# Performance work log

Measured on AMD Instinct MI355X. Metric: run time of the kernel, lower is better.

The kernel has to match this reference:

```python
import jax, jax.numpy as jnp
import numpy as np

H = 16  # num_heads
D = 1024  # hidden_size

def setup_inputs() -> dict:
    key = jax.random.key(0)
    ks = jax.random.split(key, 9)
    s = 1.0 / np.sqrt(D).astype(np.float32)
    return {
        'x':  jax.random.normal(ks[0], (2, 2048, D), dtype=jnp.float32),
        'wq': jax.random.normal(ks[1], (D, D), dtype=jnp.float32) * s,
        'bq': jax.random.normal(ks[2], (D,), dtype=jnp.float32) * s,
        'wk': jax.random.normal(ks[3], (D, D), dtype=jnp.float32) * s,
        'bk': jax.random.normal(ks[4], (D,), dtype=jnp.float32) * s,
        'wv': jax.random.normal(ks[5], (D, D), dtype=jnp.float32) * s,
        'bv': jax.random.normal(ks[6], (D,), dtype=jnp.float32) * s,
        'wo': jax.random.normal(ks[7], (D, D), dtype=jnp.float32) * s,
        'bo': jax.random.normal(ks[8], (D,), dtype=jnp.float32) * s,
    }

def _split_heads(t):
    # [b, s, (h d)] -> [b, h, s, d]
    b, s, _ = t.shape
    return t.reshape(b, s, H, D // H).transpose(0, 2, 1, 3)

def reference(x, wq, bq, wk, bk, wv, bv, wo, bo):
    q = _split_heads(x @ wq + bq)  # [b, h, s, d]
    k = _split_heads(x @ wk + bk)
    v = _split_heads(x @ wv + bv)
    scale = 1.0 / jnp.sqrt(jnp.asarray(q.shape[-1], q.dtype))
    attn = jnp.einsum('bhqd,bhkd->bhqk', q, k) * scale
    attn = jax.nn.softmax(attn, axis=-1)
    o = jnp.einsum('bhqk,bhkd->bhqd', attn, v)
    b, h, s, d = o.shape
    o = o.transpose(0, 2, 1, 3).reshape(b, s, h * d)  # concat heads
    return o @ wo + bo
```

## Files before the change

### kernel.cpp

```cpp
#include <hip/hip_runtime.h>
#include <stdint.h>
#include <stddef.h>


typedef __bf16 bf16_t;
typedef __bf16 bf16x8 __attribute__((ext_vector_type(8)));
typedef __bf16 bf16x4 __attribute__((ext_vector_type(4)));
typedef __bf16 bf16x2 __attribute__((ext_vector_type(2)));
typedef float  f32x4  __attribute__((ext_vector_type(4)));
typedef float  f32x8  __attribute__((ext_vector_type(8)));
typedef float  f32x16 __attribute__((ext_vector_type(16)));
typedef uint32_t u32x4 __attribute__((ext_vector_type(4)));

static constexpr float kQScale = 0.18033688011112042f;

__device__ __forceinline__ void gload_lds16(const bf16_t* g, bf16_t* l) {
  __builtin_amdgcn_global_load_lds((__attribute__((address_space(1))) void*)(void*)g,
                                   (__attribute__((address_space(3))) void*)l, 16, 0, 0);
}

__device__ __forceinline__ uint32_t pk_bf16(float lo, float hi) {
  bf16x2 v; v[0] = (bf16_t)lo; v[1] = (bf16_t)hi;
  return __builtin_bit_cast(uint32_t, v);
}

__global__ __launch_bounds__(256) void prep_k(
    const float* __restrict__ x, bf16_t* __restrict__ xb,
    const float* __restrict__ wq, const float* __restrict__ wk,
    const float* __restrict__ wv, const float* __restrict__ wo,
    bf16_t* __restrict__ wqkvT, bf16_t* __restrict__ woT) {
  __shared__ float t[64][65];
  const int z = blockIdx.z;
  if (z == 4) {
    const int blk = blockIdx.y * 16 + blockIdx.x;
#pragma unroll
    for (int c = 0; c < 16; ++c) {
      const int i = c * 65536 + blk * 256 + threadIdx.x;
      float4 v = ((const float4*)x)[i];
      bf16x4 o;
      o[0] = (bf16_t)v.x; o[1] = (bf16_t)v.y; o[2] = (bf16_t)v.z; o[3] = (bf16_t)v.w;
      ((bf16x4*)xb)[i] = o;
    }
    return;
  }
  const float* src = z == 0 ? wq : z == 1 ? wk : z == 2 ? wv : wo;
  bf16_t* dst = z < 3 ? wqkvT + (size_t)z * 1024 * 1024 : woT;
  int n0 = blockIdx.x * 64, k0 = blockIdx.y * 64;
  int c = threadIdx.x & 63, r4 = threadIdx.x >> 6;
#pragma unroll
  for (int i = 0; i < 16; ++i) {
    int r = r4 + i * 4;
    t[r][c] = src[(size_t)(k0 + r) * 1024 + (n0 + c)];
  }
  __syncthreads();
#pragma unroll
  for (int i = 0; i < 16; ++i) {
    int r = r4 + i * 4;
    dst[(size_t)(n0 + r) * 1024 + (k0 + c)] = (bf16_t)t[c][r];
  }
}

__global__ __launch_bounds__(256) void gemm_qkv_k(
    const bf16_t* __restrict__ A, const bf16_t* __restrict__ Bw,
    bf16_t* __restrict__ Qb, bf16_t* __restrict__ Kb, bf16_t* __restrict__ Vt,
    const float* __restrict__ bq, const float* __restrict__ bk, const float* __restrict__ bv) {
  __shared__ alignas(16) bf16_t As[128 * 32];
  __shared__ alignas(16) bf16_t Bs[128 * 32];
  const int tid = threadIdx.x;
  const int lane = tid & 63;
  const int w = tid >> 6, wr = w >> 1, wc = w & 1;
  const int brow = blockIdx.y * 128, bcol = blockIdx.x * 128;
  const int l15 = lane & 15, ko = (lane >> 4) * 8;

  f32x4 acc[4][4] = {};
  const bf16_t* Ab = A + (size_t)brow * 1024;
  const bf16_t* Bb = Bw + (size_t)bcol * 1024;

  const int e0 = tid * 8;
  const int r0 = e0 >> 5, c0 = e0 & 31;

  for (int k0 = 0; k0 < 1024; k0 += 32) {
    gload_lds16(Ab + (size_t)r0 * 1024 + k0 + c0, &As[e0]);
    gload_lds16(Ab + (size_t)(r0 + 64) * 1024 + k0 + c0, &As[e0 + 2048]);
    gload_lds16(Bb + (size_t)r0 * 1024 + k0 + c0, &Bs[e0]);
    gload_lds16(Bb + (size_t)(r0 + 64) * 1024 + k0 + c0, &Bs[e0 + 2048]);
    __syncthreads();
    bf16x8 af[4], bfg[4];
#pragma unroll
    for (int i = 0; i < 4; ++i)
      af[i] = *(const bf16x8*)&As[(wr * 64 + i * 16 + l15) * 32 + ko];
#pragma unroll
    for (int i = 0; i < 4; ++i)
      bfg[i] = *(const bf16x8*)&Bs[(wc * 64 + i * 16 + l15) * 32 + ko];
#pragma unroll
    for (int i = 0; i < 4; ++i)
#pragma unroll
      for (int j = 0; j < 4; ++j)
        acc[i][j] = __builtin_amdgcn_mfma_f32_16x16x32_bf16(af[i], bfg[j], acc[i][j], 0, 0, 0);
    __syncthreads();
  }

  const int mat = bcol >> 10;
#pragma unroll
  for (int i = 0; i < 4; ++i) {
    const int gm0 = brow + wr * 64 + i * 16 + ((lane >> 4) << 2);
    const int b = gm0 >> 11, s0 = gm0 & 2047;
#pragma unroll
    for (int j = 0; j < 4; ++j) {
      const int gn = bcol + wc * 64 + j * 16 + l15;
      const int col = gn & 1023;
      const int h = col >> 6, dd = col & 63;
      if (mat == 2) {
        const float bsv = bv[col];
        bf16x4 pk;
#pragma unroll
        for (int r = 0; r < 4; ++r) pk[r] = (bf16_t)(acc[i][j][r] + bsv);
        *(bf16x4*)&Vt[(((size_t)b * 16 + h) * 64 + dd) * 2048 + s0] = pk;
      } else {
        bf16_t* dst = mat == 0 ? Qb : Kb;
        const float bsv = (mat == 0 ? bq : bk)[col];
        const float scl = mat == 0 ? kQScale : 1.0f;
#pragma unroll
        for (int r = 0; r < 4; ++r)
          dst[((((size_t)b * 16 + h) * 2048 + (s0 + r)) * 64 + dd)] = (bf16_t)((acc[i][j][r] + bsv) * scl);
      }
    }
  }
}

__global__ __launch_bounds__(256) void gemm_out_k(
    const bf16_t* __restrict__ A, const bf16_t* __restrict__ Bw,
    float* __restrict__ outF, const float* __restrict__ bo) {
  __shared__ alignas(16) bf16_t As[128 * 32];
  __shared__ alignas(16) bf16_t Bs[64 * 32];
  const int tid = threadIdx.x;
  const int lane = tid & 63;
  const int w = tid >> 6;
  const int brow = blockIdx.y * 128, bcol = blockIdx.x * 64;
  const int l15 = lane & 15, ko = (lane >> 4) * 8;

  f32x4 acc[2][4] = {};
  const bf16_t* Ab = A + (size_t)brow * 1024;
  const bf16_t* Bb = Bw + (size_t)bcol * 1024;

  const int e0 = tid * 8;
  const int r0 = e0 >> 5, c0 = e0 & 31;

  for (int k0 = 0; k0 < 1024; k0 += 32) {
    gload_lds16(Ab + (size_t)r0 * 1024 + k0 + c0, &As[e0]);
    gload_lds16(Ab + (size_t)(r0 + 64) * 1024 + k0 + c0, &As[e0 + 2048]);
    gload_lds16(Bb + (size_t)r0 * 1024 + k0 + c0, &Bs[e0]);
    __syncthreads();
    bf16x8 af[2], bfg[4];
#pragma unroll
    for (int i = 0; i < 2; ++i)
      af[i] = *(const bf16x8*)&As[(w * 32 + i * 16 + l15) * 32 + ko];
#pragma unroll
    for (int j = 0; j < 4; ++j)
      bfg[j] = *(const bf16x8*)&Bs[(j * 16 + l15) * 32 + ko];
#pragma unroll
    for (int i = 0; i < 2; ++i)
#pragma unroll
      for (int j = 0; j < 4; ++j)
        acc[i][j] = __builtin_amdgcn_mfma_f32_16x16x32_bf16(af[i], bfg[j], acc[i][j], 0, 0, 0);
    __syncthreads();
  }

#pragma unroll
  for (int i = 0; i < 2; ++i) {
    const int gm0 = brow + w * 32 + i * 16 + ((lane >> 4) << 2);
#pragma unroll
    for (int j = 0; j < 4; ++j) {
      const int gn = bcol + j * 16 + l15;
      const float bsv = bo[gn];
#pragma unroll
      for (int r = 0; r < 4; ++r)
        outF[(size_t)(gm0 + r) * 1024 + gn] = acc[i][j][r] + bsv;
    }
  }
}

__global__ __launch_bounds__(512) void attn_k(
    const bf16_t* __restrict__ Qb, const bf16_t* __restrict__ Kb,
    const bf16_t* __restrict__ Vt, bf16_t* __restrict__ O) {
  __shared__ alignas(16) bf16_t Ksm[2][2][4096];
  __shared__ alignas(16) bf16_t Vsm[2][2][4096];
  const int tid = threadIdx.x, lane = tid & 63, w = tid >> 6;
  const int l31 = lane & 31, hi = lane >> 5;
  const int qsub = w & 3, half = w >> 2;
  const int work = (blockIdx.x & 7) * 32 + (blockIdx.x >> 3);
  const int bh = work >> 3;
  const int q0 = (work & 7) * 256 + qsub * 64;

  const bf16_t* Qp = Qb + ((size_t)bh * 2048 + q0) * 64;

  const int chunk0 = qsub * 64 + lane;
  const int srow = chunk0 >> 3;
  const int swzc = (chunk0 & 7) ^ (srow & 7);
  const char* srcK0 = (const char*)(Kb + ((size_t)bh * 2048 + half * 1024) * 64) + srow * 128 + swzc * 16;
  const char* srcK1 = srcK0 + 32 * 128;
  const char* srcV0 = (const char*)(Vt + (size_t)bh * 64 * 2048 + half * 1024) + srow * 4096 + swzc * 16;
  const char* srcV1 = srcV0 + 32 * 4096;

  auto stage = [&](int buf) {
    bf16_t* kb = &Ksm[half][buf][qsub * 512];
    bf16_t* vb = &Vsm[half][buf][qsub * 512];
    gload_lds16((const bf16_t*)srcK0, kb);
    gload_lds16((const bf16_t*)srcK1, kb + 2048);
    gload_lds16((const bf16_t*)srcV0, vb);
    gload_lds16((const bf16_t*)srcV1, vb + 2048);
    srcK0 += 8192; srcK1 += 8192;
    srcV0 += 128;  srcV1 += 128;
  };

  const int xorv = l31 & 7;
  const bf16_t* kcb[4];
#pragma unroll
  for (int j = 0; j < 4; ++j) {
    const int co = ((j * 2 + hi) ^ xorv) * 8;
    kcb[j] = &Ksm[half][0][l31 * 64 + co];
  }
  const bf16_t* vptr[8];
#pragma unroll
  for (int c = 0; c < 8; ++c)
    vptr[c] = &Vsm[half][0][l31 * 64 + ((c ^ xorv) << 3) + 4 * hi];

  bf16x8 qf[2][4];
#pragma unroll
  for (int qb = 0; qb < 2; ++qb)
#pragma unroll
    for (int ds = 0; ds < 4; ++ds)
      qf[qb][ds] = *(const bf16x8*)&Qp[(size_t)(qb * 32 + l31) * 64 + ds * 16 + hi * 8];

  f32x16 oA0 = {}, oA1 = {}, oB0 = {}, oB1 = {};
  f32x16 lsA = {}, lsB = {};
  const f32x16 kz = {};

  auto exp_pack = [&](f32x16& s0, f32x16& s1, f32x16& lsum,
                      uint32_t* pw0, uint32_t* pw1) {
#pragma unroll
    for (int r = 0; r < 16; ++r) {
      s0[r] = __builtin_amdgcn_exp2f(s0[r]);
      s1[r] = __builtin_amdgcn_exp2f(s1[r]);
    }
    lsum += s0;
    lsum += s1;
#pragma unroll
    for (int g = 0; g < 4; ++g) {
      pw0[g * 2 + 0] = pk_bf16(s0[4 * g + 0], s0[4 * g + 1]);
      pw0[g * 2 + 1] = pk_bf16(s0[4 * g + 2], s0[4 * g + 3]);
      pw1[g * 2 + 0] = pk_bf16(s1[4 * g + 0], s1[4 * g + 1]);
      pw1[g * 2 + 1] = pk_bf16(s1[4 * g + 2], s1[4 * g + 3]);
    }
  };

  auto tile_body = [&](int buf) {
    const int bo = buf * 4096;
    bf16x8 kf0[4], kf1[4];
#pragma unroll
    for (int ds = 0; ds < 4; ++ds) {
      kf0[ds] = *(const bf16x8*)(kcb[ds] + bo);
      kf1[ds] = *(const bf16x8*)(kcb[ds] + bo + 2048);
    }
    __builtin_amdgcn_s_setprio(1);
    f32x16 sA0 = __builtin_amdgcn_mfma_f32_32x32x16_bf16(kf0[0], qf[0][0], kz, 0, 0, 0);
    f32x16 sB0 = __builtin_amdgcn_mfma_f32_32x32x16_bf16(kf0[0], qf[1][0], kz, 0, 0, 0);
    f32x16 sA1 = __builtin_amdgcn_mfma_f32_32x32x16_bf16(kf1[0], qf[0][0], kz, 0, 0, 0);
    f32x16 sB1 = __builtin_amdgcn_mfma_f32_32x32x16_bf16(kf1[0], qf[1][0], kz, 0, 0, 0);
#pragma unroll
    for (int ds = 1; ds < 4; ++ds) {
      sA0 = __builtin_amdgcn_mfma_f32_32x32x16_bf16(kf0[ds], qf[0][ds], sA0, 0, 0, 0);
      sB0 = __builtin_amdgcn_mfma_f32_32x32x16_bf16(kf0[ds], qf[1][ds], sB0, 0, 0, 0);
      sA1 = __builtin_amdgcn_mfma_f32_32x32x16_bf16(kf1[ds], qf[0][ds], sA1, 0, 0, 0);
      sB1 = __builtin_amdgcn_mfma_f32_32x32x16_bf16(kf1[ds], qf[1][ds], sB1, 0, 0, 0);
    }
    __builtin_amdgcn_s_setprio(0);

    uint32_t pwA0[8], pwA1[8], pwB0[8], pwB1[8];
    exp_pack(sA0, sA1, lsA, pwA0, pwA1);
    exp_pack(sB0, sB1, lsB, pwB0, pwB1);

#pragma unroll
    for (int st = 0; st < 2; ++st) {
#pragma unroll
      for (int ks = 0; ks < 2; ++ks) {
        const bf16_t* pA = vptr[4 * st + 2 * ks] + bo;
        const bf16_t* pB = vptr[4 * st + 2 * ks + 1] + bo;
        const bf16x4 a0 = *(const bf16x4*)pA;
        const bf16x4 a1 = *(const bf16x4*)pB;
        const bf16x4 b0 = *(const bf16x4*)(pA + 2048);
        const bf16x4 b1 = *(const bf16x4*)(pB + 2048);
        const bf16x8 v0 = __builtin_shufflevector(a0, a1, 0, 1, 2, 3, 4, 5, 6, 7);
        const bf16x8 v1 = __builtin_shufflevector(b0, b1, 0, 1, 2, 3, 4, 5, 6, 7);
        const uint32_t* pwA = st ? pwA1 : pwA0;
        const uint32_t* pwB = st ? pwB1 : pwB0;
        u32x4 fa, fb;
        fa[0] = pwA[4 * ks + 0]; fa[1] = pwA[4 * ks + 1];
        fa[2] = pwA[4 * ks + 2]; fa[3] = pwA[4 * ks + 3];
        fb[0] = pwB[4 * ks + 0]; fb[1] = pwB[4 * ks + 1];
        fb[2] = pwB[4 * ks + 2]; fb[3] = pwB[4 * ks + 3];
        const bf16x8 pfA = __builtin_bit_cast(bf16x8, fa);
        const bf16x8 pfB = __builtin_bit_cast(bf16x8, fb);
        __builtin_amdgcn_s_setprio(1);
        oA0 = __builtin_amdgcn_mfma_f32_32x32x16_bf16(v0, pfA, oA0, 0, 0, 0);
        oA1 = __builtin_amdgcn_mfma_f32_32x32x16_bf16(v1, pfA, oA1, 0, 0, 0);
        oB0 = __builtin_amdgcn_mfma_f32_32x32x16_bf16(v0, pfB, oB0, 0, 0, 0);
        oB1 = __builtin_amdgcn_mfma_f32_32x32x16_bf16(v1, pfB, oB1, 0, 0, 0);
        __builtin_amdgcn_s_setprio(0);
      }
    }
  };

  stage(0);
  __syncthreads();
#pragma unroll 1
  for (int t = 0; t < 16; t += 2) {
    stage(1);
    tile_body(0);
    __syncthreads();
    if (t + 2 < 16) stage(0);
    tile_body(1);
    if (t + 2 < 16) __syncthreads();
  }

  auto red16 = [](const f32x16& v) {
    f32x8 a = __builtin_shufflevector(v, v, 0, 1, 2, 3, 4, 5, 6, 7) +
              __builtin_shufflevector(v, v, 8, 9, 10, 11, 12, 13, 14, 15);
    f32x4 b = __builtin_shufflevector(a, a, 0, 1, 2, 3) +
              __builtin_shufflevector(a, a, 4, 5, 6, 7);
    return (b[0] + b[1]) + (b[2] + b[3]);
  };
  float liA = red16(lsA); liA += __shfl_xor(liA, 32);
  float liB = red16(lsB); liB += __shfl_xor(liB, 32);

  __syncthreads();
  float* cmb_o = (float*)&Ksm[0][0][0];
  float* cmb_l = (float*)&Vsm[0][0][0];
  const int b = bh >> 4, h = bh & 15;

  if (half) {
    cmb_l[(0 * 4 + qsub) * 64 + lane] = liA;
    cmb_l[(1 * 4 + qsub) * 64 + lane] = liB;
#pragma unroll
    for (int r = 0; r < 16; ++r) {
      cmb_o[(qsub * 32 + r) * 64 + lane] = oA0[r];
      cmb_o[(qsub * 32 + 16 + r) * 64 + lane] = oA1[r];
    }
  }
  __syncthreads();
  if (!half) {
    const float inv = 1.0f / (liA + cmb_l[(0 * 4 + qsub) * 64 + lane]);
    const size_t row = (size_t)b * 2048 + q0 + l31;
#pragma unroll
    for (int g = 0; g < 4; ++g) {
      bf16x4 p0, p1;
#pragma unroll
      for (int r = 0; r < 4; ++r) {
        p0[r] = (bf16_t)((oA0[4 * g + r] + cmb_o[(qsub * 32 + 4 * g + r) * 64 + lane]) * inv);
        p1[r] = (bf16_t)((oA1[4 * g + r] + cmb_o[(qsub * 32 + 16 + 4 * g + r) * 64 + lane]) * inv);
      }
      *(bf16x4*)&O[row * 1024 + h * 64 + 0  + g * 8 + hi * 4] = p0;
      *(bf16x4*)&O[row * 1024 + h * 64 + 32 + g * 8 + hi * 4] = p1;
    }
  }
  __syncthreads();
  if (half) {
#pragma unroll
    for (int r = 0; r < 16; ++r) {
      cmb_o[(qsub * 32 + r) * 64 + lane] = oB0[r];
      cmb_o[(qsub * 32 + 16 + r) * 64 + lane] = oB1[r];
    }
  }
  __syncthreads();
  if (!half) {
    const float inv = 1.0f / (liB + cmb_l[(1 * 4 + qsub) * 64 + lane]);
    const size_t row = (size_t)b * 2048 + q0 + 32 + l31;
#pragma unroll
    for (int g = 0; g < 4; ++g) {
      bf16x4 p0, p1;
#pragma unroll
      for (int r = 0; r < 4; ++r) {
        p0[r] = (bf16_t)((oB0[4 * g + r] + cmb_o[(qsub * 32 + 4 * g + r) * 64 + lane]) * inv);
        p1[r] = (bf16_t)((oB1[4 * g + r] + cmb_o[(qsub * 32 + 16 + 4 * g + r) * 64 + lane]) * inv);
      }
      *(bf16x4*)&O[row * 1024 + h * 64 + 0  + g * 8 + hi * 4] = p0;
      *(bf16x4*)&O[row * 1024 + h * 64 + 32 + g * 8 + hi * 4] = p1;
    }
  }
}

extern "C" void kernel_launch(void* const* d_in, const int* in_sizes, int n_in,
                              void* d_out, int out_size, void* d_ws, size_t ws_size,
                              hipStream_t stream) {
  const float* x  = (const float*)d_in[0];
  const float* wq = (const float*)d_in[1];
  const float* bq = (const float*)d_in[2];
  const float* wk = (const float*)d_in[3];
  const float* bk = (const float*)d_in[4];
  const float* wv = (const float*)d_in[5];
  const float* bv = (const float*)d_in[6];
  const float* wo = (const float*)d_in[7];
  const float* bo = (const float*)d_in[8];
  float* out = (float*)d_out;

  if (ws_size < ((size_t)48 << 20)) return;
  char* ws = (char*)d_ws;
  bf16_t* xb  = (bf16_t*)(ws);
  bf16_t* wT  = (bf16_t*)(ws + ((size_t)8 << 20));
  bf16_t* woT = wT + (size_t)3072 * 1024;
  bf16_t* Qb  = (bf16_t*)(ws + ((size_t)16 << 20));
  bf16_t* Kb  = (bf16_t*)(ws + ((size_t)24 << 20));
  bf16_t* Vt  = (bf16_t*)(ws + ((size_t)32 << 20));
  bf16_t* O   = xb;

  prep_k<<<dim3(16, 16, 5), 256, 0, stream>>>(x, xb, wq, wk, wv, wo, wT, woT);
  gemm_qkv_k<<<dim3(24, 32), 256, 0, stream>>>(xb, wT, Qb, Kb, Vt, bq, bk, bv);
  attn_k<<<256, 512, 0, stream>>>(Qb, Kb, Vt, O);
  gemm_out_k<<<dim3(16, 32), 256, 0, stream>>>(O, woT, out, bo);
}
```

Before: 119.1 us.

## Double KV tile size per stage and process subtiles sequentially in attention

Each pipeline stage now loads 128 keys/values per half instead of 64, with a 16-chunk V row layout, halving the number of main-loop iterations and barriers. The tile body handles four 32-key subtiles one at a time, computing scores, exp and PV for each before moving on. The row sum is reduced to a scalar per subtile instead of kept in a 16-wide vector accumulator, which lowers register pressure at the cost of more scalar adds. LDS use doubles, which may reduce occupancy.

```diff
diff --git a/kernel.cpp b/kernel.cpp
--- a/kernel.cpp
+++ b/kernel.cpp
@@ -183,8 +183,8 @@
 __global__ __launch_bounds__(512) void attn_k(
     const bf16_t* __restrict__ Qb, const bf16_t* __restrict__ Kb,
     const bf16_t* __restrict__ Vt, bf16_t* __restrict__ O) {
-  __shared__ alignas(16) bf16_t Ksm[2][2][4096];
-  __shared__ alignas(16) bf16_t Vsm[2][2][4096];
+  __shared__ alignas(16) bf16_t Ksm[2][2][8192];
+  __shared__ alignas(16) bf16_t Vsm[2][2][8192];
   const int tid = threadIdx.x, lane = tid & 63, w = tid >> 6;
   const int l31 = lane & 31, hi = lane >> 5;
   const int qsub = w & 3, half = w >> 2;
@@ -194,36 +194,36 @@
 
   const bf16_t* Qp = Qb + ((size_t)bh * 2048 + q0) * 64;
 
-  const int chunk0 = qsub * 64 + lane;
-  const int srow = chunk0 >> 3;
-  const int swzc = (chunk0 & 7) ^ (srow & 7);
-  const char* srcK0 = (const char*)(Kb + ((size_t)bh * 2048 + half * 1024) * 64) + srow * 128 + swzc * 16;
-  const char* srcK1 = srcK0 + 32 * 128;
-  const char* srcV0 = (const char*)(Vt + (size_t)bh * 64 * 2048 + half * 1024) + srow * 4096 + swzc * 16;
-  const char* srcV1 = srcV0 + 32 * 4096;
+  const int t256 = qsub * 64 + lane;
+  const int krow = t256 >> 3, kc = (t256 & 7) ^ (krow & 7);
+  const char* srcK0 = (const char*)(Kb + ((size_t)bh * 2048 + half * 1024) * 64) + krow * 128 + kc * 16;
+  const int vrow = t256 >> 4, vc = (t256 & 15) ^ (vrow & 7);
+  const char* srcV0 = (const char*)(Vt + (size_t)bh * 64 * 2048 + half * 1024) + vrow * 4096 + vc * 16;
 
   auto stage = [&](int buf) {
     bf16_t* kb = &Ksm[half][buf][qsub * 512];
     bf16_t* vb = &Vsm[half][buf][qsub * 512];
-    gload_lds16((const bf16_t*)srcK0, kb);
-    gload_lds16((const bf16_t*)srcK1, kb + 2048);
-    gload_lds16((const bf16_t*)srcV0, vb);
-    gload_lds16((const bf16_t*)srcV1, vb + 2048);
-    srcK0 += 8192; srcK1 += 8192;
-    srcV0 += 128;  srcV1 += 128;
+    gload_lds16((const bf16_t*)(srcK0), kb);
+    gload_lds16((const bf16_t*)(srcK0 + 4096), kb + 2048);
+    gload_lds16((const bf16_t*)(srcK0 + 8192), kb + 4096);
+    gload_lds16((const bf16_t*)(srcK0 + 12288), kb + 6144);
+    gload_lds16((const bf16_t*)(srcV0), vb);
+    gload_lds16((const bf16_t*)(srcV0 + 65536), vb + 2048);
+    gload_lds16((const bf16_t*)(srcV0 + 131072), vb + 4096);
+    gload_lds16((const bf16_t*)(srcV0 + 196608), vb + 6144);
+    srcK0 += 16384;
+    srcV0 += 256;
   };
 
   const int xorv = l31 & 7;
   const bf16_t* kcb[4];
 #pragma unroll
-  for (int j = 0; j < 4; ++j) {
-    const int co = ((j * 2 + hi) ^ xorv) * 8;
-    kcb[j] = &Ksm[half][0][l31 * 64 + co];
-  }
+  for (int j = 0; j < 4; ++j)
+    kcb[j] = &Ksm[half][0][l31 * 64 + ((j * 2 + hi) ^ xorv) * 8];
   const bf16_t* vptr[8];
 #pragma unroll
   for (int c = 0; c < 8; ++c)
-    vptr[c] = &Vsm[half][0][l31 * 64 + ((c ^ xorv) << 3) + 4 * hi];
+    vptr[c] = &Vsm[half][0][l31 * 128 + ((c ^ xorv) << 3) + 4 * hi];
 
   bf16x8 qf[2][4];
 #pragma unroll
@@ -233,67 +233,62 @@
       qf[qb][ds] = *(const bf16x8*)&Qp[(size_t)(qb * 32 + l31) * 64 + ds * 16 + hi * 8];
 
   f32x16 oA0 = {}, oA1 = {}, oB0 = {}, oB1 = {};
-  f32x16 lsA = {}, lsB = {};
+  float liA = 0.0f, liB = 0.0f;
   const f32x16 kz = {};
 
-  auto exp_pack = [&](f32x16& s0, f32x16& s1, f32x16& lsum,
-                      uint32_t* pw0, uint32_t* pw1) {
-#pragma unroll
-    for (int r = 0; r < 16; ++r) {
-      s0[r] = __builtin_amdgcn_exp2f(s0[r]);
-      s1[r] = __builtin_amdgcn_exp2f(s1[r]);
-    }
-    lsum += s0;
-    lsum += s1;
-#pragma unroll
-    for (int g = 0; g < 4; ++g) {
-      pw0[g * 2 + 0] = pk_bf16(s0[4 * g + 0], s0[4 * g + 1]);
-      pw0[g * 2 + 1] = pk_bf16(s0[4 * g + 2], s0[4 * g + 3]);
-      pw1[g * 2 + 0] = pk_bf16(s1[4 * g + 0], s1[4 * g + 1]);
-      pw1[g * 2 + 1] = pk_bf16(s1[4 * g + 2], s1[4 * g + 3]);
-    }
+  auto red16 = [](const f32x16& v) {
+    f32x8 a = __builtin_shufflevector(v, v, 0, 1, 2, 3, 4, 5, 6, 7) +
+              __builtin_shufflevector(v, v, 8, 9, 10, 11, 12, 13, 14, 15);
+    f32x4 b = __builtin_shufflevector(a, a, 0, 1, 2, 3) +
+              __builtin_shufflevector(a, a, 4, 5, 6, 7);
+    return (b[0] + b[1]) + (b[2] + b[3]);
   };
 
   auto tile_body = [&](int buf) {
-    const int bo = buf * 4096;
-    bf16x8 kf0[4], kf1[4];
-#pragma unroll
-    for (int ds = 0; ds < 4; ++ds) {
-      kf0[ds] = *(const bf16x8*)(kcb[ds] + bo);
-      kf1[ds] = *(const bf16x8*)(kcb[ds] + bo + 2048);
-    }
-    __builtin_amdgcn_s_setprio(1);
-    f32x16 sA0 = __builtin_amdgcn_mfma_f32_32x32x16_bf16(kf0[0], qf[0][0], kz, 0, 0, 0);
-    f32x16 sB0 = __builtin_amdgcn_mfma_f32_32x32x16_bf16(kf0[0], qf[1][0], kz, 0, 0, 0);
-    f32x16 sA1 = __builtin_amdgcn_mfma_f32_32x32x16_bf16(kf1[0], qf[0][0], kz, 0, 0, 0);
-    f32x16 sB1 = __builtin_amdgcn_mfma_f32_32x32x16_bf16(kf1[0], qf[1][0], kz, 0, 0, 0);
-#pragma unroll
-    for (int ds = 1; ds < 4; ++ds) {
-      sA0 = __builtin_amdgcn_mfma_f32_32x32x16_bf16(kf0[ds], qf[0][ds], sA0, 0, 0, 0);
-      sB0 = __builtin_amdgcn_mfma_f32_32x32x16_bf16(kf0[ds], qf[1][ds], sB0, 0, 0, 0);
-      sA1 = __builtin_amdgcn_mfma_f32_32x32x16_bf16(kf1[ds], qf[0][ds], sA1, 0, 0, 0);
-      sB1 = __builtin_amdgcn_mfma_f32_32x32x16_bf16(kf1[ds], qf[1][ds], sB1, 0, 0, 0);
-    }
-    __builtin_amdgcn_s_setprio(0);
-
-    uint32_t pwA0[8], pwA1[8], pwB0[8], pwB1[8];
-    exp_pack(sA0, sA1, lsA, pwA0, pwA1);
-    exp_pack(sB0, sB1, lsB, pwB0, pwB1);
-
-#pragma unroll
-    for (int st = 0; st < 2; ++st) {
+    const int bo = buf * 8192;
+#pragma unroll
+    for (int st = 0; st < 4; ++st) {
+      bf16x8 kf[4];
+#pragma unroll
+      for (int ds = 0; ds < 4; ++ds)
+        kf[ds] = *(const bf16x8*)(kcb[ds] + bo + st * 2048);
+      __builtin_amdgcn_s_setprio(1);
+      f32x16 sA = __builtin_amdgcn_mfma_f32_32x32x16_bf16(kf[0], qf[0][0], kz, 0, 0, 0);
+      f32x16 sB = __builtin_amdgcn_mfma_f32_32x32x16_bf16(kf[0], qf[1][0], kz, 0, 0, 0);
+#pragma unroll
+      for (int ds = 1; ds < 4; ++ds) {
+        sA = __builtin_amdgcn_mfma_f32_32x32x16_bf16(kf[ds], qf[0][ds], sA, 0, 0, 0);
+        sB = __builtin_amdgcn_mfma_f32_32x32x16_bf16(kf[ds], qf[1][ds], sB, 0, 0, 0);
+      }
+      __builtin_amdgcn_s_setprio(0);
+
+#pragma unroll
+      for (int r = 0; r < 16; ++r) {
+        sA[r] = __builtin_amdgcn_exp2f(sA[r]);
+        sB[r] = __builtin_amdgcn_exp2f(sB[r]);
+      }
+      liA += red16(sA);
+      liB += red16(sB);
+      uint32_t pwA[8], pwB[8];
+#pragma unroll
+      for (int g = 0; g < 4; ++g) {
+        pwA[g * 2 + 0] = pk_bf16(sA[4 * g + 0], sA[4 * g + 1]);
+        pwA[g * 2 + 1] = pk_bf16(sA[4 * g + 2], sA[4 * g + 3]);
+        pwB[g * 2 + 0] = pk_bf16(sB[4 * g + 0], sB[4 * g + 1]);
+        pwB[g * 2 + 1] = pk_bf16(sB[4 * g + 2], sB[4 * g + 3]);
+      }
+
 #pragma unroll
       for (int ks = 0; ks < 2; ++ks) {
-        const bf16_t* pA = vptr[4 * st + 2 * ks] + bo;
-        const bf16_t* pB = vptr[4 * st + 2 * ks + 1] + bo;
+        const int c0i = st * 4 + 2 * ks;
+        const bf16_t* pA = vptr[c0i & 7] + ((c0i & 8) ? 64 : 0) + bo;
+        const bf16_t* pB = vptr[(c0i + 1) & 7] + (((c0i + 1) & 8) ? 64 : 0) + bo;
         const bf16x4 a0 = *(const bf16x4*)pA;
         const bf16x4 a1 = *(const bf16x4*)pB;
-        const bf16x4 b0 = *(const bf16x4*)(pA + 2048);
-        const bf16x4 b1 = *(const bf16x4*)(pB + 2048);
+        const bf16x4 b0 = *(const bf16x4*)(pA + 4096);
+        const bf16x4 b1 = *(const bf16x4*)(pB + 4096);
         const bf16x8 v0 = __builtin_shufflevector(a0, a1, 0, 1, 2, 3, 4, 5, 6, 7);
         const bf16x8 v1 = __builtin_shufflevector(b0, b1, 0, 1, 2, 3, 4, 5, 6, 7);
-        const uint32_t* pwA = st ? pwA1 : pwA0;
-        const uint32_t* pwB = st ? pwB1 : pwB0;
         u32x4 fa, fb;
         fa[0] = pwA[4 * ks + 0]; fa[1] = pwA[4 * ks + 1];
         fa[2] = pwA[4 * ks + 2]; fa[3] = pwA[4 * ks + 3];
@@ -314,24 +309,17 @@
   stage(0);
   __syncthreads();
 #pragma unroll 1
-  for (int t = 0; t < 16; t += 2) {
+  for (int t = 0; t < 8; t += 2) {
     stage(1);
     tile_body(0);
     __syncthreads();
-    if (t + 2 < 16) stage(0);
+    if (t + 2 < 8) stage(0);
     tile_body(1);
-    if (t + 2 < 16) __syncthreads();
-  }
-
-  auto red16 = [](const f32x16& v) {
-    f32x8 a = __builtin_shufflevector(v, v, 0, 1, 2, 3, 4, 5, 6, 7) +
-              __builtin_shufflevector(v, v, 8, 9, 10, 11, 12, 13, 14, 15);
-    f32x4 b = __builtin_shufflevector(a, a, 0, 1, 2, 3) +
-              __builtin_shufflevector(a, a, 4, 5, 6, 7);
-    return (b[0] + b[1]) + (b[2] + b[3]);
-  };
-  float liA = red16(lsA); liA += __shfl_xor(liA, 32);
-  float liB = red16(lsB); liB += __shfl_xor(liB, 32);
+    if (t + 2 < 8) __syncthreads();
+  }
+
+  liA += __shfl_xor(liA, 32);
+  liB += __shfl_xor(liB, 32);
 
   __syncthreads();
   float* cmb_o = (float*)&Ksm[0][0][0];
```

Result: slower. 122.5 us (+2.9%).
